# Kernel tuning notes

Measured on AMD Instinct MI355X. Metric: run time of the kernel, lower is better.

## Reference

```python
import jax, jax.numpy as jnp
import numpy as np

H = 1024
HEADS = 16
FFN = 4096
EPS = 1e-5


def _layernorm(x, g, b):
    mu = jnp.mean(x, axis=-1, keepdims=True)
    var = jnp.mean((x - mu) ** 2, axis=-1, keepdims=True)
    return (x - mu) * jax.lax.rsqrt(var + EPS) * g + b


def setup_inputs() -> dict:
    key = jax.random.key(0)
    ks = jax.random.split(key, 12)
    N, L = 2, 2048
    s = 1.0 / np.sqrt(H)
    inp = {
        "src_hidden": jax.random.normal(ks[0], (N, L, H), dtype=jnp.float32),
        "key_mask": jnp.ones((N, L), dtype=jnp.int32),
        "Wq": jax.random.normal(ks[1], (H, H), dtype=jnp.float32) * s,
        "bq": jnp.zeros((H,), dtype=jnp.float32),
        "Wk": jax.random.normal(ks[2], (H, H), dtype=jnp.float32) * s,
        "bk": jnp.zeros((H,), dtype=jnp.float32),
        "Wv": jax.random.normal(ks[3], (H, H), dtype=jnp.float32) * s,
        "bv": jnp.zeros((H,), dtype=jnp.float32),
        "Wo": jax.random.normal(ks[4], (H, H), dtype=jnp.float32) * s,
        "bo": jnp.zeros((H,), dtype=jnp.float32),
        "ln1_g": jnp.ones((H,), dtype=jnp.float32),
        "ln1_b": jnp.zeros((H,), dtype=jnp.float32),
        "W1": jax.random.normal(ks[5], (H, FFN), dtype=jnp.float32) * s,
        "b1": jnp.zeros((FFN,), dtype=jnp.float32),
        "W2": jax.random.normal(ks[6], (FFN, H), dtype=jnp.float32) * (1.0 / np.sqrt(FFN)),
        "b2": jnp.zeros((H,), dtype=jnp.float32),
        "ln2_g": jnp.ones((H,), dtype=jnp.float32),
        "ln2_b": jnp.zeros((H,), dtype=jnp.float32),
    }
    return inp


def reference(src_hidden, key_mask, Wq, bq, Wk, bk, Wv, bv, Wo, bo,
              ln1_g, ln1_b, W1, b1, W2, b2, ln2_g, ln2_b):
    N, L, _ = src_hidden.shape
    d = H // HEADS
    # projections -> (N, heads, L, d)
    q = (src_hidden @ Wq + bq).reshape(N, L, HEADS, d).transpose(0, 2, 1, 3)
    k = (src_hidden @ Wk + bk).reshape(N, L, HEADS, d).transpose(0, 2, 1, 3)
    v = (src_hidden @ Wv + bv).reshape(N, L, HEADS, d).transpose(0, 2, 1, 3)
    # faithful quirk: Q/=sqrt(H) and K/=sqrt(H)  =>  scores scaled by 1/H
    sims = jnp.einsum('bhid,bhjd->bhij', q, k) / H  # (N, heads, L, L)
    mask = key_mask[:, None, None, :] != 0          # (N,1,1,L), masked=False
    sims = jnp.where(mask, sims, -jnp.inf)
    attn = jax.nn.softmax(sims, axis=-1)
    ctx = jnp.einsum('bhij,bhjd->bhid', attn, v)
    concats = ctx.transpose(0, 2, 1, 3).reshape(N, L, H)
    mhsa = concats @ Wo + bo
    # residual + LN1
    x = _layernorm(mhsa + src_hidden, ln1_g, ln1_b)
    # FFN (dropout=0 / eval) + residual + LN2
    ffn = jax.nn.relu(x @ W1 + b1) @ W2 + b2
    out = _layernorm(ffn + x, ln2_g, ln2_b)
    return out
```

## Files before the change

### kernel.cpp

```cpp
#include <hip/hip_runtime.h>
#include <math.h>

#define Hd   1024
#define SEQL 2048
#define NB   2
#define NHEADS 16
#define FFND 4096
#define ROWS 4096
#define QKVLD 3072

typedef __attribute__((ext_vector_type(8))) short short8;
typedef __attribute__((ext_vector_type(4))) float f32x4;

__device__ __forceinline__ unsigned short f2bf(float f) {
  union { float f; unsigned int u; } v; v.f = f;
  return (unsigned short)((v.u + 0x7fffu + ((v.u >> 16) & 1u)) >> 16);
}
__device__ __forceinline__ unsigned short f2bf_fast(float f) {
  union { float f; unsigned int u; } v; v.f = f;
  return (unsigned short)((v.u + 0x8000u) >> 16);
}
__device__ __forceinline__ float bf2f(unsigned short u) {
  union { unsigned int u; float f; } v; v.u = (unsigned int)u << 16;
  return v.f;
}

__device__ __forceinline__ void gl_lds16(const unsigned short* g,
                                         unsigned short* l) {
  __builtin_amdgcn_global_load_lds(
      (const __attribute__((address_space(1))) void*)g,
      (__attribute__((address_space(3))) void*)l, 16, 0, 0);
}

__global__ __launch_bounds__(256) void convert_bf16(
    const float* __restrict__ in, unsigned short* __restrict__ out) {
  const int i = (blockIdx.x * 256 + threadIdx.x) * 4;
  float4 x = *(const float4*)&in[i];
  ushort4 o;
  o.x = f2bf(x.x); o.y = f2bf(x.y); o.z = f2bf(x.z); o.w = f2bf(x.w);
  *(ushort4*)&out[i] = o;
}

__global__ __launch_bounds__(256) void convert_transpose(
    const float* __restrict__ W, int ld,
    unsigned short* __restrict__ Wt, int ldt) {
  __shared__ float T[64][65];
  const int t = threadIdx.x;
  const int c0 = blockIdx.x * 64, r0 = blockIdx.y * 64;
#pragma unroll
  for (int p = 0; p < 4; ++p) {
    const int lin = t + p * 256;
    const int r = lin >> 4, c4 = (lin & 15) * 4;
    float4 x = *(const float4*)&W[(size_t)(r0 + r) * ld + c0 + c4];
    T[r][c4 + 0] = x.x; T[r][c4 + 1] = x.y;
    T[r][c4 + 2] = x.z; T[r][c4 + 3] = x.w;
  }
  __syncthreads();
#pragma unroll
  for (int p = 0; p < 2; ++p) {
    const int lin = t + p * 256;
    const int oc = lin >> 3, ch = (lin & 7) * 8;
    union { unsigned short u[8]; uint4 v; } x;
#pragma unroll
    for (int i = 0; i < 8; ++i) x.u[i] = f2bf(T[ch + i][oc]);
    *(uint4*)&Wt[(size_t)(c0 + oc) * ldt + r0 + ch] = x.v;
  }
}

__global__ __launch_bounds__(256) void convert_transpose4(
    const float* __restrict__ W0, const float* __restrict__ W1,
    const float* __restrict__ W2, const float* __restrict__ W3,
    unsigned short* __restrict__ T0, unsigned short* __restrict__ T1,
    unsigned short* __restrict__ T2, unsigned short* __restrict__ T3) {
  __shared__ float T[64][65];
  const float* W = (blockIdx.z == 0) ? W0 : (blockIdx.z == 1) ? W1
                 : (blockIdx.z == 2) ? W2 : W3;
  unsigned short* Wt = (blockIdx.z == 0) ? T0 : (blockIdx.z == 1) ? T1
                     : (blockIdx.z == 2) ? T2 : T3;
  const int t = threadIdx.x;
  const int c0 = blockIdx.x * 64, r0 = blockIdx.y * 64;
#pragma unroll
  for (int p = 0; p < 4; ++p) {
    const int lin = t + p * 256;
    const int r = lin >> 4, c4 = (lin & 15) * 4;
    float4 x = *(const float4*)&W[(size_t)(r0 + r) * Hd + c0 + c4];
    T[r][c4 + 0] = x.x; T[r][c4 + 1] = x.y;
    T[r][c4 + 2] = x.z; T[r][c4 + 3] = x.w;
  }
  __syncthreads();
#pragma unroll
  for (int p = 0; p < 2; ++p) {
    const int lin = t + p * 256;
    const int oc = lin >> 3, ch = (lin & 7) * 8;
    union { unsigned short u[8]; uint4 v; } x;
#pragma unroll
    for (int i = 0; i < 8; ++i) x.u[i] = f2bf(T[ch + i][oc]);
    *(uint4*)&Wt[(size_t)(c0 + oc) * Hd + r0 + ch] = x.v;
  }
}

__global__ __launch_bounds__(256) void concat3(
    const float* __restrict__ a, const float* __restrict__ b,
    const float* __restrict__ c, float* __restrict__ o) {
  const int i = blockIdx.x * 256 + threadIdx.x;
  o[i] = (i < 1024) ? a[i] : (i < 2048 ? b[i - 1024] : c[i - 2048]);
}

__global__ __launch_bounds__(256) void transpose_v(
    const unsigned short* __restrict__ v, unsigned short* __restrict__ vt) {
  __shared__ unsigned short T[64][72];
  const int t = threadIdx.x;
  const int s0 = (blockIdx.x & 31) * 64;
  const int bh = blockIdx.x >> 5;
  const int b = bh >> 4, h = bh & 15;
#pragma unroll
  for (int p = 0; p < 2; ++p) {
    const int lin = t + p * 256;
    const int r = lin >> 3, c8 = (lin & 7) * 8;
    *(uint4*)&T[r][c8] =
        *(const uint4*)&v[(size_t)(b * SEQL + s0 + r) * QKVLD + h * 64 + c8];
  }
  __syncthreads();
#pragma unroll
  for (int p = 0; p < 2; ++p) {
    const int lin = t + p * 256;
    const int d = lin >> 3, c8 = (lin & 7) * 8;
    union { unsigned short u[8]; uint4 v4; } x;
#pragma unroll
    for (int i = 0; i < 8; ++i) x.u[i] = T[c8 + i][d];
    *(uint4*)&vt[(size_t)(bh * 64 + d) * SEQL + s0 + c8] = x.v4;
  }
}

template <int BN, int MODE, int OUTBF>
__global__ __launch_bounds__(256, (BN == 128 ? 3 : 4)) void gemm_bt(
    const unsigned short* __restrict__ A, int lda,
    const unsigned short* __restrict__ Bt, int ldb,
    const float* __restrict__ bias,
    void* __restrict__ Cv, int ldc, int K) {
  constexpr int NI = (BN == 128) ? 4 : 2;
  constexpr int BG = BN / 32;
  __shared__ unsigned short As[128 * 64];
  __shared__ unsigned short Bs[BN * 64];
  const int t = threadIdx.x;
  const int wave = t >> 6, lane = t & 63;
  const int l16 = lane & 15, quad = lane >> 4;
  const int m0 = blockIdx.y * 128, n0 = blockIdx.x * BN;
  const int wm = (wave >> 1) * 64, wn = (wave & 1) * (BN / 2);

  const int lr8 = lane >> 3;
  const int sc8 = 8 * ((lane & 7) ^ lr8);

  f32x4 acc[4][NI];
#pragma unroll
  for (int i = 0; i < 4; ++i)
#pragma unroll
    for (int j = 0; j < NI; ++j) acc[i][j] = (f32x4){0.f, 0.f, 0.f, 0.f};

  const unsigned short* Apg[4];
  unsigned short* lAg[4];
#pragma unroll
  for (int j = 0; j < 4; ++j) {
    const int r0 = (wave + 4 * j) * 8;
    Apg[j] = &A[(size_t)(m0 + r0 + lr8) * lda + sc8];
    lAg[j] = &As[r0 * 64];
  }
  const unsigned short* Bpg[BG];
  unsigned short* lBg[BG];
#pragma unroll
  for (int j = 0; j < BG; ++j) {
    const int r0 = (wave + 4 * j) * 8;
    Bpg[j] = &Bt[(size_t)(n0 + r0 + lr8) * ldb + sc8];
    lBg[j] = &Bs[r0 * 64];
  }

  for (int k0 = 0; k0 < K; k0 += 64) {
#pragma unroll
    for (int j = 0; j < 4; ++j) gl_lds16(Apg[j] + k0, lAg[j]);
#pragma unroll
    for (int j = 0; j < BG; ++j) gl_lds16(Bpg[j] + k0, lBg[j]);
    __syncthreads();

#pragma unroll
    for (int kh = 0; kh < 2; ++kh) {
      short8 af[4], bfr[NI];
#pragma unroll
      for (int mi = 0; mi < 4; ++mi) {
        const int r = wm + mi * 16 + l16;
        af[mi] = *(const short8*)&As[r * 64 + (((quad + 4 * kh) ^ (r & 7)) * 8)];
      }
#pragma unroll
      for (int ni = 0; ni < NI; ++ni) {
        const int r = wn + ni * 16 + l16;
        bfr[ni] = *(const short8*)&Bs[r * 64 + (((quad + 4 * kh) ^ (r & 7)) * 8)];
      }
#pragma unroll
      for (int mi = 0; mi < 4; ++mi)
#pragma unroll
        for (int ni = 0; ni < NI; ++ni)
          acc[mi][ni] = __builtin_amdgcn_mfma_f32_16x16x32_bf16(
              af[mi], bfr[ni], acc[mi][ni], 0, 0, 0);
    }
    __syncthreads();
  }

#pragma unroll
  for (int mi = 0; mi < 4; ++mi) {
#pragma unroll
    for (int ni = 0; ni < NI; ++ni) {
      const int col = n0 + wn + ni * 16 + l16;
      const float bv = (MODE == 2) ? 0.0f : bias[col];
#pragma unroll
      for (int r = 0; r < 4; ++r) {
        const int row = m0 + wm + mi * 16 + quad * 4 + r;
        float v = acc[mi][ni][r] + bv;
        if (MODE == 1) v = fmaxf(v, 0.0f);
        if (OUTBF) {
          ((unsigned short*)Cv)[(size_t)row * ldc + col] = f2bf_fast(v);
        } else {
          float* Cf = (float*)Cv;
          if (MODE == 2) Cf[(size_t)row * ldc + col] += v;
          else           Cf[(size_t)row * ldc + col] = v;
        }
      }
    }
  }
}

__global__ __launch_bounds__(256, 5) void attn_mfma(
    const unsigned short* __restrict__ Q,
    const unsigned short* __restrict__ K,
    const unsigned short* __restrict__ Vt,
    const int* __restrict__ mask,
    unsigned short* __restrict__ Op,
    float* __restrict__ ls) {
  __shared__ unsigned short Qs[64 * 72];
  __shared__ unsigned short Ks[64 * 72];
  __shared__ unsigned short Vs[64 * 72];
  unsigned short* Ps = Qs;

  const int t = threadIdx.x;
  const int wave = t >> 6, lane = t & 63;
  const int l16 = lane & 15, quad = lane >> 4;
  const int qb = blockIdx.x & 31;
  const int h  = (blockIdx.x >> 5) & 15;
  const int b  = (blockIdx.x >> 9) & 1;
  const int jh = blockIdx.x >> 10;
  const int q0 = qb * 64;
  const int bh = b * NHEADS + h;
  const int jbeg = jh * (SEQL / 2), jend = jbeg + SEQL / 2;
  const float NEGINF = -__builtin_inff();

  const int lr = t >> 3, lc8 = (t & 7) * 8;
  const unsigned short* Kbase = &K[(size_t)(b * SEQL + lr) * QKVLD + h * 64 + lc8];
  const unsigned short* Vbase = &Vt[(size_t)(bh * 64 + lr) * SEQL + lc8];
  const size_t Krow32 = (size_t)32 * QKVLD;

#pragma unroll
  for (int p = 0; p < 2; ++p) {
    const int r = lr + p * 32;
    *(uint4*)&Qs[r * 72 + lc8] =
        *(const uint4*)&Q[(size_t)(b * SEQL + q0 + r) * QKVLD + h * 64 + lc8];
  }
  __syncthreads();
  const short8 aq0 = *(const short8*)&Qs[(wave * 16 + l16) * 72 + quad * 8];
  const short8 aq1 = *(const short8*)&Qs[(wave * 16 + l16) * 72 + 32 + quad * 8];

  float lrow[4] = {0.f, 0.f, 0.f, 0.f};
  f32x4 accO[4];
#pragma unroll
  for (int nd = 0; nd < 4; ++nd) accO[nd] = (f32x4){0.f, 0.f, 0.f, 0.f};

  uint4 kv0 = *(const uint4*)(Kbase + (size_t)jbeg * QKVLD);
  uint4 kv1 = *(const uint4*)(Kbase + (size_t)jbeg * QKVLD + Krow32);
  uint4 vv0 = *(const uint4*)(Vbase + jbeg);
  uint4 vv1 = *(const uint4*)(Vbase + jbeg + 32 * SEQL);

  for (int j0 = jbeg; j0 < jend; j0 += 64) {
    __syncthreads();
    *(uint4*)&Ks[lr * 72 + lc8] = kv0;
    *(uint4*)&Ks[(lr + 32) * 72 + lc8] = kv1;
    *(uint4*)&Vs[lr * 72 + lc8] = vv0;
    *(uint4*)&Vs[(lr + 32) * 72 + lc8] = vv1;
    __syncthreads();

    if (j0 + 64 < jend) {
      const unsigned short* kp = Kbase + (size_t)(j0 + 64) * QKVLD;
      const unsigned short* vp = Vbase + (j0 + 64);
      kv0 = *(const uint4*)(kp);
      kv1 = *(const uint4*)(kp + Krow32);
      vv0 = *(const uint4*)(vp);
      vv1 = *(const uint4*)(vp + 32 * SEQL);
    }

#pragma unroll
    for (int nt = 0; nt < 4; ++nt) {
      short8 bk0 = *(const short8*)&Ks[(nt * 16 + l16) * 72 + quad * 8];
      short8 bk1 = *(const short8*)&Ks[(nt * 16 + l16) * 72 + 32 + quad * 8];
      f32x4 z = (f32x4){0.f, 0.f, 0.f, 0.f};
      z = __builtin_amdgcn_mfma_f32_16x16x32_bf16(aq0, bk0, z, 0, 0, 0);
      z = __builtin_amdgcn_mfma_f32_16x16x32_bf16(aq1, bk1, z, 0, 0, 0);
      const bool ok = mask[b * SEQL + j0 + nt * 16 + l16] != 0;
      unsigned short pk[4];
#pragma unroll
      for (int r = 0; r < 4; ++r) {
        const float x = ok ? z[r] * (1.0f / 1024.0f) : NEGINF;
        const float p = __expf(x);
        lrow[r] += p;
        pk[r] = f2bf_fast(p);
      }
#pragma unroll
      for (int r = 0; r < 4; ++r)
        Ps[(wave * 16 + quad * 4 + r) * 72 + nt * 16 + l16] = pk[r];
    }

    short8 ap0 = *(const short8*)&Ps[(wave * 16 + l16) * 72 + quad * 8];
    short8 ap1 = *(const short8*)&Ps[(wave * 16 + l16) * 72 + 32 + quad * 8];
#pragma unroll
    for (int nd = 0; nd < 4; ++nd) {
      short8 bv0 = *(const short8*)&Vs[(nd * 16 + l16) * 72 + quad * 8];
      short8 bv1 = *(const short8*)&Vs[(nd * 16 + l16) * 72 + 32 + quad * 8];
      accO[nd] = __builtin_amdgcn_mfma_f32_16x16x32_bf16(ap0, bv0, accO[nd], 0, 0, 0);
      accO[nd] = __builtin_amdgcn_mfma_f32_16x16x32_bf16(ap1, bv1, accO[nd], 0, 0, 0);
    }
  }

#pragma unroll
  for (int r = 0; r < 4; ++r) {
#pragma unroll
    for (int off = 1; off < 16; off <<= 1)
      lrow[r] += __shfl_xor(lrow[r], off, 64);
  }
  if (l16 == 0) {
#pragma unroll
    for (int r = 0; r < 4; ++r)
      ls[((size_t)(jh * NB + b) * NHEADS + h) * SEQL + q0 + wave * 16 +
         quad * 4 + r] = lrow[r];
  }
#pragma unroll
  for (int nd = 0; nd < 4; ++nd)
#pragma unroll
    for (int r = 0; r < 4; ++r) {
      const int rowg = b * SEQL + q0 + wave * 16 + quad * 4 + r;
      Op[(size_t)jh * ROWS * Hd + (size_t)rowg * Hd + h * 64 + nd * 16 + l16] =
          f2bf_fast(accO[nd][r]);
    }
}

__global__ __launch_bounds__(256) void attn_combine(
    const unsigned short* __restrict__ Op, const float* __restrict__ ls,
    unsigned short* __restrict__ ctxb) {
  const int row = blockIdx.x;
  const int b = row >> 11, q = row & (SEQL - 1);
  const int t = threadIdx.x;
  const int c0 = t * 4, h = t >> 4;
  const float l0 = ls[((size_t)(b)*NHEADS + h) * SEQL + q];
  const float l1 = ls[((size_t)(NB + b) * NHEADS + h) * SEQL + q];
  const float inv = 1.0f / (l0 + l1);
  ushort4 a = *(const ushort4*)&Op[(size_t)row * Hd + c0];
  ushort4 c = *(const ushort4*)&Op[(size_t)ROWS * Hd + (size_t)row * Hd + c0];
  ushort4 o;
  o.x = f2bf_fast((bf2f(a.x) + bf2f(c.x)) * inv);
  o.y = f2bf_fast((bf2f(a.y) + bf2f(c.y)) * inv);
  o.z = f2bf_fast((bf2f(a.z) + bf2f(c.z)) * inv);
  o.w = f2bf_fast((bf2f(a.w) + bf2f(c.w)) * inv);
  *(ushort4*)&ctxb[(size_t)row * Hd + c0] = o;
}

template <int ABF>
__global__ __launch_bounds__(256) void add_ln_kernel(
    const void* Av, const float* R,
    const float* __restrict__ gamma, const float* __restrict__ beta,
    float* out, unsigned short* outb) {
  const int row = blockIdx.x;
  const int t = threadIdx.x;
  const size_t baser = (size_t)row * Hd;

  float a0, a1, a2, a3;
  if (ABF) {
    ushort4 a = *(const ushort4*)&((const unsigned short*)Av)[baser + t * 4];
    a0 = bf2f(a.x); a1 = bf2f(a.y); a2 = bf2f(a.z); a3 = bf2f(a.w);
  } else {
    float4 a = *(const float4*)&((const float*)Av)[baser + t * 4];
    a0 = a.x; a1 = a.y; a2 = a.z; a3 = a.w;
  }
  float4 r = *(const float4*)&R[baser + t * 4];
  float x0 = a0 + r.x, x1 = a1 + r.y, x2 = a2 + r.z, x3 = a3 + r.w;
  float s  = x0 + x1 + x2 + x3;
  float ss = x0 * x0 + x1 * x1 + x2 * x2 + x3 * x3;

#pragma unroll
  for (int off = 32; off > 0; off >>= 1) {
    s  += __shfl_down(s, off, 64);
    ss += __shfl_down(ss, off, 64);
  }

  __shared__ float rs[4], rss[4];
  __shared__ float sh_mean, sh_rstd;
  if ((t & 63) == 0) { rs[t >> 6] = s; rss[t >> 6] = ss; }
  __syncthreads();
  if (t == 0) {
    const float S  = rs[0] + rs[1] + rs[2] + rs[3];
    const float SS = rss[0] + rss[1] + rss[2] + rss[3];
    const float mean = S * (1.0f / Hd);
    const float var  = SS * (1.0f / Hd) - mean * mean;
    sh_mean = mean;
    sh_rstd = rsqrtf(var + 1e-5f);
  }
  __syncthreads();
  const float mean = sh_mean, rstd = sh_rstd;

  float4 gm = *(const float4*)&gamma[t * 4];
  float4 bt = *(const float4*)&beta[t * 4];
  float4 o;
  o.x = (x0 - mean) * rstd * gm.x + bt.x;
  o.y = (x1 - mean) * rstd * gm.y + bt.y;
  o.z = (x2 - mean) * rstd * gm.z + bt.z;
  o.w = (x3 - mean) * rstd * gm.w + bt.w;
  *(float4*)&out[baser + t * 4] = o;
  if (outb) {
    ushort4 ob;
    ob.x = f2bf(o.x); ob.y = f2bf(o.y); ob.z = f2bf(o.z); ob.w = f2bf(o.w);
    *(ushort4*)&outb[baser + t * 4] = ob;
  }
}

extern "C" void kernel_launch(void* const* d_in, const int* in_sizes, int n_in,
                              void* d_out, int out_size, void* d_ws, size_t ws_size,
                              hipStream_t stream) {
  const float* src  = (const float*)d_in[0];
  const int*   kmsk = (const int*)  d_in[1];
  const float* Wq   = (const float*)d_in[2];
  const float* bq   = (const float*)d_in[3];
  const float* Wk   = (const float*)d_in[4];
  const float* bk   = (const float*)d_in[5];
  const float* Wv   = (const float*)d_in[6];
  const float* bv   = (const float*)d_in[7];
  const float* Wo   = (const float*)d_in[8];
  const float* bo   = (const float*)d_in[9];
  const float* ln1g = (const float*)d_in[10];
  const float* ln1b = (const float*)d_in[11];
  const float* W1   = (const float*)d_in[12];
  const float* b1   = (const float*)d_in[13];
  const float* W2   = (const float*)d_in[14];
  const float* b2   = (const float*)d_in[15];
  const float* ln2g = (const float*)d_in[16];
  const float* ln2b = (const float*)d_in[17];

  char* w8 = (char*)d_ws;
  char* o8 = (char*)d_out;
  const size_t MB = 1024 * 1024;
  unsigned short* srcb  = (unsigned short*)(w8 + 0 * MB);
  unsigned short* WqkvT = (unsigned short*)(w8 + 8 * MB);
  float*          bqkv  = (float*)(w8 + 14 * MB);
  unsigned short* qkv   = (unsigned short*)(w8 + 16 * MB);
  unsigned short* vt    = (unsigned short*)(w8 + 40 * MB);
  unsigned short* Opart = (unsigned short*)(w8 + 0 * MB);
  float*          ls    = (float*)(o8 + 8 * MB);
  unsigned short* WoT   = (unsigned short*)(o8 + 9 * MB);
  unsigned short* ctxb  = (unsigned short*)d_out;
  float*          mhsa  = (float*)(w8 + 16 * MB);
  float*          x1    = (float*)d_out;
  unsigned short* x1b   = (unsigned short*)(w8 + 8 * MB);
  unsigned short* W1T   = (unsigned short*)(w8 + 0 * MB);
  unsigned short* hb    = (unsigned short*)(w8 + 16 * MB);
  unsigned short* W2T   = (unsigned short*)(w8 + 0 * MB);
  unsigned short* f2b   = (unsigned short*)(w8 + 8 * MB);

  dim3 blk(256);

  convert_bf16<<<ROWS * Hd / 1024, blk, 0, stream>>>(src, srcb);
  convert_transpose4<<<dim3(16, 16, 4), blk, 0, stream>>>(
      Wq, Wk, Wv, Wo, WqkvT, WqkvT + 1024 * 1024, WqkvT + 2 * 1024 * 1024, WoT);
  concat3<<<12, blk, 0, stream>>>(bq, bk, bv, bqkv);

  gemm_bt<128, 0, 1><<<dim3(QKVLD / 128, ROWS / 128), blk, 0, stream>>>(
      srcb, Hd, WqkvT, Hd, bqkv, qkv, QKVLD, Hd);

  transpose_v<<<1024, blk, 0, stream>>>(qkv + 2048, vt);
  attn_mfma<<<2048, blk, 0, stream>>>(qkv, qkv + 1024, vt, kmsk, Opart, ls);
  attn_combine<<<ROWS, blk, 0, stream>>>(Opart, ls, ctxb);

  gemm_bt<64, 0, 0><<<dim3(Hd / 64, ROWS / 128), blk, 0, stream>>>(
      ctxb, Hd, WoT, Hd, bo, mhsa, Hd, Hd);

  add_ln_kernel<0><<<ROWS, blk, 0, stream>>>(mhsa, src, ln1g, ln1b, x1, x1b);

  convert_transpose<<<dim3(64, 16), blk, 0, stream>>>(W1, FFND, W1T, Hd);
  gemm_bt<128, 1, 1><<<dim3(FFND / 128, ROWS / 128), blk, 0, stream>>>(
      x1b, Hd, W1T, Hd, b1, hb, FFND, Hd);
  convert_transpose<<<dim3(16, 64), blk, 0, stream>>>(W2, Hd, W2T, FFND);
  gemm_bt<64, 0, 1><<<dim3(Hd / 64, ROWS / 128), blk, 0, stream>>>(
      hb, FFND, W2T, FFND, b2, f2b, Hd, FFND);

  add_ln_kernel<1><<<ROWS, blk, 0, stream>>>(f2b, x1, ln2g, ln2b,
                                             (float*)d_out, nullptr);
}
```

Before: 387.4 us.

## Double-buffer GEMM LDS tiles and fold bias concat into convert kernel

```diff
diff --git a/kernel.cpp b/kernel.cpp
--- a/kernel.cpp
+++ b/kernel.cpp
@@ -33,12 +33,20 @@
 }
 
 __global__ __launch_bounds__(256) void convert_bf16(
-    const float* __restrict__ in, unsigned short* __restrict__ out) {
-  const int i = (blockIdx.x * 256 + threadIdx.x) * 4;
+    const float* __restrict__ in, unsigned short* __restrict__ out,
+    const float* __restrict__ a, const float* __restrict__ b,
+    const float* __restrict__ c, float* __restrict__ o) {
+  const int bid = blockIdx.x;
+  if (bid >= ROWS * Hd / 1024) {
+    const int i = (bid - ROWS * Hd / 1024) * 256 + threadIdx.x;
+    o[i] = (i < 1024) ? a[i] : (i < 2048 ? b[i - 1024] : c[i - 2048]);
+    return;
+  }
+  const int i = (bid * 256 + threadIdx.x) * 4;
   float4 x = *(const float4*)&in[i];
-  ushort4 o;
-  o.x = f2bf(x.x); o.y = f2bf(x.y); o.z = f2bf(x.z); o.w = f2bf(x.w);
-  *(ushort4*)&out[i] = o;
+  ushort4 ov;
+  ov.x = f2bf(x.x); ov.y = f2bf(x.y); ov.z = f2bf(x.z); ov.w = f2bf(x.w);
+  *(ushort4*)&out[i] = ov;
 }
 
 __global__ __launch_bounds__(256) void convert_transpose(
@@ -99,13 +107,6 @@
   }
 }
 
-__global__ __launch_bounds__(256) void concat3(
-    const float* __restrict__ a, const float* __restrict__ b,
-    const float* __restrict__ c, float* __restrict__ o) {
-  const int i = blockIdx.x * 256 + threadIdx.x;
-  o[i] = (i < 1024) ? a[i] : (i < 2048 ? b[i - 1024] : c[i - 2048]);
-}
-
 __global__ __launch_bounds__(256) void transpose_v(
     const unsigned short* __restrict__ v, unsigned short* __restrict__ vt) {
   __shared__ unsigned short T[64][72];
@@ -133,15 +134,15 @@
 }
 
 template <int BN, int MODE, int OUTBF>
-__global__ __launch_bounds__(256, (BN == 128 ? 3 : 4)) void gemm_bt(
+__global__ __launch_bounds__(256, (BN == 128 ? 2 : 3)) void gemm_bt(
     const unsigned short* __restrict__ A, int lda,
     const unsigned short* __restrict__ Bt, int ldb,
     const float* __restrict__ bias,
     void* __restrict__ Cv, int ldc, int K) {
   constexpr int NI = (BN == 128) ? 4 : 2;
   constexpr int BG = BN / 32;
-  __shared__ unsigned short As[128 * 64];
-  __shared__ unsigned short Bs[BN * 64];
+  __shared__ unsigned short As[2][128 * 64];
+  __shared__ unsigned short Bs[2][BN * 64];
   const int t = threadIdx.x;
   const int wave = t >> 6, lane = t & 63;
   const int l16 = lane & 15, quad = lane >> 4;
@@ -158,28 +159,40 @@
     for (int j = 0; j < NI; ++j) acc[i][j] = (f32x4){0.f, 0.f, 0.f, 0.f};
 
   const unsigned short* Apg[4];
-  unsigned short* lAg[4];
+  int lAo[4];
 #pragma unroll
   for (int j = 0; j < 4; ++j) {
     const int r0 = (wave + 4 * j) * 8;
     Apg[j] = &A[(size_t)(m0 + r0 + lr8) * lda + sc8];
-    lAg[j] = &As[r0 * 64];
+    lAo[j] = r0 * 64;
   }
   const unsigned short* Bpg[BG];
-  unsigned short* lBg[BG];
+  int lBo[BG];
 #pragma unroll
   for (int j = 0; j < BG; ++j) {
     const int r0 = (wave + 4 * j) * 8;
     Bpg[j] = &Bt[(size_t)(n0 + r0 + lr8) * ldb + sc8];
-    lBg[j] = &Bs[r0 * 64];
-  }
-
-  for (int k0 = 0; k0 < K; k0 += 64) {
-#pragma unroll
-    for (int j = 0; j < 4; ++j) gl_lds16(Apg[j] + k0, lAg[j]);
-#pragma unroll
-    for (int j = 0; j < BG; ++j) gl_lds16(Bpg[j] + k0, lBg[j]);
+    lBo[j] = r0 * 64;
+  }
+
+  const int NT = K >> 6;
+
+#pragma unroll
+  for (int j = 0; j < 4; ++j) gl_lds16(Apg[j], &As[0][lAo[j]]);
+#pragma unroll
+  for (int j = 0; j < BG; ++j) gl_lds16(Bpg[j], &Bs[0][lBo[j]]);
+
+  for (int tk = 0; tk < NT; ++tk) {
+    const int cb = tk & 1, nb = cb ^ 1;
     __syncthreads();
+
+    if (tk + 1 < NT) {
+      const int k1 = (tk + 1) << 6;
+#pragma unroll
+      for (int j = 0; j < 4; ++j) gl_lds16(Apg[j] + k1, &As[nb][lAo[j]]);
+#pragma unroll
+      for (int j = 0; j < BG; ++j) gl_lds16(Bpg[j] + k1, &Bs[nb][lBo[j]]);
+    }
 
 #pragma unroll
     for (int kh = 0; kh < 2; ++kh) {
@@ -187,12 +200,12 @@
 #pragma unroll
       for (int mi = 0; mi < 4; ++mi) {
         const int r = wm + mi * 16 + l16;
-        af[mi] = *(const short8*)&As[r * 64 + (((quad + 4 * kh) ^ (r & 7)) * 8)];
+        af[mi] = *(const short8*)&As[cb][r * 64 + (((quad + 4 * kh) ^ (r & 7)) * 8)];
       }
 #pragma unroll
       for (int ni = 0; ni < NI; ++ni) {
         const int r = wn + ni * 16 + l16;
-        bfr[ni] = *(const short8*)&Bs[r * 64 + (((quad + 4 * kh) ^ (r & 7)) * 8)];
+        bfr[ni] = *(const short8*)&Bs[cb][r * 64 + (((quad + 4 * kh) ^ (r & 7)) * 8)];
       }
 #pragma unroll
       for (int mi = 0; mi < 4; ++mi)
@@ -201,7 +214,6 @@
           acc[mi][ni] = __builtin_amdgcn_mfma_f32_16x16x32_bf16(
               af[mi], bfr[ni], acc[mi][ni], 0, 0, 0);
     }
-    __syncthreads();
   }
 
 #pragma unroll
@@ -469,10 +481,10 @@
 
   dim3 blk(256);
 
-  convert_bf16<<<ROWS * Hd / 1024, blk, 0, stream>>>(src, srcb);
+  convert_bf16<<<ROWS * Hd / 1024 + 12, blk, 0, stream>>>(
+      src, srcb, bq, bk, bv, bqkv);
   convert_transpose4<<<dim3(16, 16, 4), blk, 0, stream>>>(
       Wq, Wk, Wv, Wo, WqkvT, WqkvT + 1024 * 1024, WqkvT + 2 * 1024 * 1024, WoT);
-  concat3<<<12, blk, 0, stream>>>(bq, bk, bv, bqkv);
 
   gemm_bt<128, 0, 1><<<dim3(QKVLD / 128, ROWS / 128), blk, 0, stream>>>(
       srcb, Hd, WqkvT, Hd, bqkv, qkv, QKVLD, Hd);
```

Result: no change. 389.5 us (+0.5%).

## Rework attention to 32x32 MFMA with register-resident P via permlane swap

Applied to the files above, without the earlier changes.

```diff
diff --git a/kernel.cpp b/kernel.cpp
--- a/kernel.cpp
+++ b/kernel.cpp
@@ -11,6 +11,7 @@
 
 typedef __attribute__((ext_vector_type(8))) short short8;
 typedef __attribute__((ext_vector_type(4))) float f32x4;
+typedef __attribute__((ext_vector_type(16))) float f32x16;
 
 __device__ __forceinline__ unsigned short f2bf(float f) {
   union { float f; unsigned int u; } v; v.f = f;
@@ -23,6 +24,14 @@
 __device__ __forceinline__ float bf2f(unsigned short u) {
   union { unsigned int u; float f; } v; v.u = (unsigned int)u << 16;
   return v.f;
+}
+__device__ __forceinline__ int cvtpk(float a, float b) {
+  int d;
+  asm("v_cvt_pk_bf16_f32 %0, %1, %2" : "=v"(d) : "v"(a), "v"(b));
+  return d;
+}
+__device__ __forceinline__ void pswap(int& a, int& b) {
+  asm("v_permlane32_swap_b32 %0, %1" : "+v"(a), "+v"(b));
 }
 
 __device__ __forceinline__ void gl_lds16(const unsigned short* g,
@@ -33,12 +42,20 @@
 }
 
 __global__ __launch_bounds__(256) void convert_bf16(
-    const float* __restrict__ in, unsigned short* __restrict__ out) {
-  const int i = (blockIdx.x * 256 + threadIdx.x) * 4;
+    const float* __restrict__ in, unsigned short* __restrict__ out,
+    const float* __restrict__ a, const float* __restrict__ b,
+    const float* __restrict__ c, float* __restrict__ o) {
+  const int bid = blockIdx.x;
+  if (bid >= ROWS * Hd / 1024) {
+    const int i = (bid - ROWS * Hd / 1024) * 256 + threadIdx.x;
+    o[i] = (i < 1024) ? a[i] : (i < 2048 ? b[i - 1024] : c[i - 2048]);
+    return;
+  }
+  const int i = (bid * 256 + threadIdx.x) * 4;
   float4 x = *(const float4*)&in[i];
-  ushort4 o;
-  o.x = f2bf(x.x); o.y = f2bf(x.y); o.z = f2bf(x.z); o.w = f2bf(x.w);
-  *(ushort4*)&out[i] = o;
+  ushort4 ov;
+  ov.x = f2bf(x.x); ov.y = f2bf(x.y); ov.z = f2bf(x.z); ov.w = f2bf(x.w);
+  *(ushort4*)&out[i] = ov;
 }
 
 __global__ __launch_bounds__(256) void convert_transpose(
@@ -97,13 +114,6 @@
     for (int i = 0; i < 8; ++i) x.u[i] = f2bf(T[ch + i][oc]);
     *(uint4*)&Wt[(size_t)(c0 + oc) * Hd + r0 + ch] = x.v;
   }
-}
-
-__global__ __launch_bounds__(256) void concat3(
-    const float* __restrict__ a, const float* __restrict__ b,
-    const float* __restrict__ c, float* __restrict__ o) {
-  const int i = blockIdx.x * 256 + threadIdx.x;
-  o[i] = (i < 1024) ? a[i] : (i < 2048 ? b[i - 1024] : c[i - 2048]);
 }
 
 __global__ __launch_bounds__(256) void transpose_v(
@@ -227,26 +237,24 @@
   }
 }
 
-__global__ __launch_bounds__(256, 5) void attn_mfma(
+__global__ __launch_bounds__(256, 4) void attn_mfma(
     const unsigned short* __restrict__ Q,
     const unsigned short* __restrict__ K,
     const unsigned short* __restrict__ Vt,
     const int* __restrict__ mask,
     unsigned short* __restrict__ Op,
     float* __restrict__ ls) {
-  __shared__ unsigned short Qs[64 * 72];
   __shared__ unsigned short Ks[64 * 72];
   __shared__ unsigned short Vs[64 * 72];
-  unsigned short* Ps = Qs;
 
   const int t = threadIdx.x;
   const int wave = t >> 6, lane = t & 63;
-  const int l16 = lane & 15, quad = lane >> 4;
-  const int qb = blockIdx.x & 31;
-  const int h  = (blockIdx.x >> 5) & 15;
-  const int b  = (blockIdx.x >> 9) & 1;
-  const int jh = blockIdx.x >> 10;
-  const int q0 = qb * 64;
+  const int l32 = lane & 31, hi = lane >> 5;
+  const int qb = blockIdx.x & 15;
+  const int h  = (blockIdx.x >> 4) & 15;
+  const int b  = (blockIdx.x >> 8) & 1;
+  const int jh = blockIdx.x >> 9;
+  const int q0 = qb * 128;
   const int bh = b * NHEADS + h;
   const int jbeg = jh * (SEQL / 2), jend = jbeg + SEQL / 2;
   const float NEGINF = -__builtin_inff();
@@ -256,20 +264,19 @@
   const unsigned short* Vbase = &Vt[(size_t)(bh * 64 + lr) * SEQL + lc8];
   const size_t Krow32 = (size_t)32 * QKVLD;
 
-#pragma unroll
-  for (int p = 0; p < 2; ++p) {
-    const int r = lr + p * 32;
-    *(uint4*)&Qs[r * 72 + lc8] =
-        *(const uint4*)&Q[(size_t)(b * SEQL + q0 + r) * QKVLD + h * 64 + lc8];
-  }
-  __syncthreads();
-  const short8 aq0 = *(const short8*)&Qs[(wave * 16 + l16) * 72 + quad * 8];
-  const short8 aq1 = *(const short8*)&Qs[(wave * 16 + l16) * 72 + 32 + quad * 8];
-
-  float lrow[4] = {0.f, 0.f, 0.f, 0.f};
-  f32x4 accO[4];
-#pragma unroll
-  for (int nd = 0; nd < 4; ++nd) accO[nd] = (f32x4){0.f, 0.f, 0.f, 0.f};
+  const unsigned short* Qrow =
+      &Q[(size_t)(b * SEQL + q0 + wave * 32 + l32) * QKVLD + h * 64];
+  short8 qf[4];
+#pragma unroll
+  for (int ks = 0; ks < 4; ++ks)
+    qf[ks] = *(const short8*)&Qrow[ks * 16 + hi * 8];
+
+  float lrow = 0.f;
+  f32x16 accO[2];
+#pragma unroll
+  for (int dt = 0; dt < 2; ++dt)
+#pragma unroll
+    for (int r = 0; r < 16; ++r) accO[dt][r] = 0.f;
 
   uint4 kv0 = *(const uint4*)(Kbase + (size_t)jbeg * QKVLD);
   uint4 kv1 = *(const uint4*)(Kbase + (size_t)jbeg * QKVLD + Krow32);
@@ -294,56 +301,66 @@
     }
 
 #pragma unroll
-    for (int nt = 0; nt < 4; ++nt) {
-      short8 bk0 = *(const short8*)&Ks[(nt * 16 + l16) * 72 + quad * 8];
-      short8 bk1 = *(const short8*)&Ks[(nt * 16 + l16) * 72 + 32 + quad * 8];
-      f32x4 z = (f32x4){0.f, 0.f, 0.f, 0.f};
-      z = __builtin_amdgcn_mfma_f32_16x16x32_bf16(aq0, bk0, z, 0, 0, 0);
-      z = __builtin_amdgcn_mfma_f32_16x16x32_bf16(aq1, bk1, z, 0, 0, 0);
-      const bool ok = mask[b * SEQL + j0 + nt * 16 + l16] != 0;
-      unsigned short pk[4];
-#pragma unroll
-      for (int r = 0; r < 4; ++r) {
-        const float x = ok ? z[r] * (1.0f / 1024.0f) : NEGINF;
-        const float p = __expf(x);
-        lrow[r] += p;
-        pk[r] = f2bf_fast(p);
+    for (int jt = 0; jt < 2; ++jt) {
+      f32x16 z;
+#pragma unroll
+      for (int r = 0; r < 16; ++r) z[r] = 0.f;
+#pragma unroll
+      for (int ks = 0; ks < 4; ++ks) {
+        const short8 ka =
+            *(const short8*)&Ks[(jt * 32 + l32) * 72 + ks * 16 + hi * 8];
+        z = __builtin_amdgcn_mfma_f32_32x32x16_bf16(ka, qf[ks], z, 0, 0, 0);
       }
-#pragma unroll
-      for (int r = 0; r < 4; ++r)
-        Ps[(wave * 16 + quad * 4 + r) * 72 + nt * 16 + l16] = pk[r];
+
+      int pk[8];
+#pragma unroll
+      for (int g = 0; g < 4; ++g) {
+        const int4 mm =
+            *(const int4*)&mask[b * SEQL + j0 + jt * 32 + g * 8 + hi * 4];
+        const int mr[4] = {mm.x, mm.y, mm.z, mm.w};
+        float p[4];
+#pragma unroll
+        for (int e = 0; e < 4; ++e) {
+          const float x = mr[e] ? z[g * 4 + e] * (1.0f / 1024.0f) : NEGINF;
+          p[e] = __expf(x);
+          lrow += p[e];
+        }
+        pk[g * 2 + 0] = cvtpk(p[0], p[1]);
+        pk[g * 2 + 1] = cvtpk(p[2], p[3]);
+      }
+      pswap(pk[0], pk[2]); pswap(pk[1], pk[3]);
+      pswap(pk[4], pk[6]); pswap(pk[5], pk[7]);
+      union { int i[4]; short8 s; } pa0, pa1;
+      pa0.i[0] = pk[0]; pa0.i[1] = pk[1]; pa0.i[2] = pk[2]; pa0.i[3] = pk[3];
+      pa1.i[0] = pk[4]; pa1.i[1] = pk[5]; pa1.i[2] = pk[6]; pa1.i[3] = pk[7];
+
+#pragma unroll
+      for (int dt = 0; dt < 2; ++dt) {
+        const short8 vb0 = *(const short8*)&Vs[(dt * 32 + l32) * 72 +
+                                               jt * 32 + hi * 8];
+        const short8 vb1 = *(const short8*)&Vs[(dt * 32 + l32) * 72 +
+                                               jt * 32 + 16 + hi * 8];
+        accO[dt] = __builtin_amdgcn_mfma_f32_32x32x16_bf16(pa0.s, vb0,
+                                                           accO[dt], 0, 0, 0);
+        accO[dt] = __builtin_amdgcn_mfma_f32_32x32x16_bf16(pa1.s, vb1,
+                                                           accO[dt], 0, 0, 0);
+      }
     }
-
-    short8 ap0 = *(const short8*)&Ps[(wave * 16 + l16) * 72 + quad * 8];
-    short8 ap1 = *(const short8*)&Ps[(wave * 16 + l16) * 72 + 32 + quad * 8];
-#pragma unroll
-    for (int nd = 0; nd < 4; ++nd) {
-      short8 bv0 = *(const short8*)&Vs[(nd * 16 + l16) * 72 + quad * 8];
-      short8 bv1 = *(const short8*)&Vs[(nd * 16 + l16) * 72 + 32 + quad * 8];
-      accO[nd] = __builtin_amdgcn_mfma_f32_16x16x32_bf16(ap0, bv0, accO[nd], 0, 0, 0);
-      accO[nd] = __builtin_amdgcn_mfma_f32_16x16x32_bf16(ap1, bv1, accO[nd], 0, 0, 0);
-    }
-  }
-
-#pragma unroll
-  for (int r = 0; r < 4; ++r) {
-#pragma unroll
-    for (int off = 1; off < 16; off <<= 1)
-      lrow[r] += __shfl_xor(lrow[r], off, 64);
-  }
-  if (l16 == 0) {
-#pragma unroll
-    for (int r = 0; r < 4; ++r)
-      ls[((size_t)(jh * NB + b) * NHEADS + h) * SEQL + q0 + wave * 16 +
-         quad * 4 + r] = lrow[r];
-  }
-#pragma unroll
-  for (int nd = 0; nd < 4; ++nd)
-#pragma unroll
-    for (int r = 0; r < 4; ++r) {
-      const int rowg = b * SEQL + q0 + wave * 16 + quad * 4 + r;
-      Op[(size_t)jh * ROWS * Hd + (size_t)rowg * Hd + h * 64 + nd * 16 + l16] =
-          f2bf_fast(accO[nd][r]);
+  }
+
+  lrow += __shfl_xor(lrow, 32);
+  if (hi == 0)
+    ls[((size_t)(jh * NB + b) * NHEADS + h) * SEQL + q0 + wave * 32 + l32] =
+        lrow;
+
+#pragma unroll
+  for (int dt = 0; dt < 2; ++dt)
+#pragma unroll
+    for (int r = 0; r < 16; ++r) {
+      const int qr = q0 + wave * 32 + (r & 3) + 8 * (r >> 2) + 4 * hi;
+      const int rowg = b * SEQL + qr;
+      Op[(size_t)jh * ROWS * Hd + (size_t)rowg * Hd + h * 64 + dt * 32 + l32] =
+          f2bf_fast(accO[dt][r]);
     }
 }
 
@@ -469,16 +486,16 @@
 
   dim3 blk(256);
 
-  convert_bf16<<<ROWS * Hd / 1024, blk, 0, stream>>>(src, srcb);
+  convert_bf16<<<ROWS * Hd / 1024 + 12, blk, 0, stream>>>(
+      src, srcb, bq, bk, bv, bqkv);
   convert_transpose4<<<dim3(16, 16, 4), blk, 0, stream>>>(
       Wq, Wk, Wv, Wo, WqkvT, WqkvT + 1024 * 1024, WqkvT + 2 * 1024 * 1024, WoT);
-  concat3<<<12, blk, 0, stream>>>(bq, bk, bv, bqkv);
 
   gemm_bt<128, 0, 1><<<dim3(QKVLD / 128, ROWS / 128), blk, 0, stream>>>(
       srcb, Hd, WqkvT, Hd, bqkv, qkv, QKVLD, Hd);
 
   transpose_v<<<1024, blk, 0, stream>>>(qkv + 2048, vt);
-  attn_mfma<<<2048, blk, 0, stream>>>(qkv, qkv + 1024, vt, kmsk, Opart, ls);
+  attn_mfma<<<1024, blk, 0, stream>>>(qkv, qkv + 1024, vt, kmsk, Opart, ls);
   attn_combine<<<ROWS, blk, 0, stream>>>(Opart, ls, ctxb);
 
   gemm_bt<64, 0, 0><<<dim3(Hd / 64, ROWS / 128), blk, 0, stream>>>(
```

Measured after the change: 378.6 us. 2.3% less time.
